# Performance work log

Hardware: AMD Instinct MI355X
Metric: run time of the kernel (lower is better)

## Reference

```python
import jax, jax.numpy as jnp
import numpy as np
from jax import lax

# Shared Conv2d [1,1] + BN + ReLU is represented as a per-point affine (BN folded
# into conv weight/bias at eval) followed by ReLU, matching inference-mode math.

B, N1, N2, K = 8, 8192, 2048, 8
C1, C2 = 64, 128
MLP0, MLP1, MLP2 = 128, 128, 128  # mlp=[128,128], mlp2=[128]


def setup_inputs() -> dict:
    key = jax.random.key(0)
    ks = jax.random.split(key, 10)
    sc = lambda fan_in: 1.0 / np.sqrt(fan_in)
    return {
        "xyz1": jax.random.normal(ks[0], (B, N1, 3), jnp.float32),
        "xyz2": jax.random.normal(ks[1], (B, N2, 3), jnp.float32),
        "feat1": jax.random.normal(ks[2], (B, N1, C1), jnp.float32),
        "feat2": jax.random.normal(ks[3], (B, N2, C2), jnp.float32),
        "W0": jax.random.normal(ks[4], (C2 + 3, MLP0), jnp.float32) * sc(C2 + 3),
        "b0": jnp.zeros((MLP0,), jnp.float32),
        "W1": jax.random.normal(ks[5], (MLP0, MLP1), jnp.float32) * sc(MLP0),
        "b1": jnp.zeros((MLP1,), jnp.float32),
        "W2": jax.random.normal(ks[6], (MLP1 + C1, MLP2), jnp.float32) * sc(MLP1 + C1),
        "b2": jnp.zeros((MLP2,), jnp.float32),
    }


def _knn_idx(xyz1, xyz2, k):
    # squared distances (B, N1, N2); top-k nearest in xyz2 for each xyz1 point
    d2 = jnp.sum((xyz1[:, :, None, :] - xyz2[:, None, :, :]) ** 2, axis=-1)
    _, idx = lax.top_k(-d2, k)  # (B, N1, K)
    return idx


def _gather(src, idx):
    # src: (B, N2, C), idx: (B, N1, K) -> (B, N1, K, C)
    return jax.vmap(lambda s, i: s[i])(src, idx)


def reference(xyz1, xyz2, feat1, feat2, W0, b0, W1, b1, W2, b2):
    idx = _knn_idx(xyz1, xyz2, K)
    xyz2_g = _gather(xyz2, idx)            # (B, N1, K, 3)
    feat2_g = _gather(feat2, idx)          # (B, N1, K, C2)
    xyz_diff = xyz2_g - xyz1[:, :, None, :]
    net = jnp.concatenate([feat2_g, xyz_diff], axis=-1)  # (B, N1, K, C2+3)
    net = jax.nn.relu(net @ W0 + b0)
    net = jax.nn.relu(net @ W1 + b1)       # (B, N1, K, MLP1)
    pooled = jnp.max(net, axis=2)          # max pooling over neighbors
    cat = jnp.concatenate([pooled, feat1], axis=-1)      # (B, N1, MLP1+C1)
    out = jax.nn.relu(cat @ W2 + b2)       # (B, N1, MLP2)
    return out
```

## Files before the change

### kernel.cpp

```cpp
#include <hip/hip_runtime.h>
#include <hip/hip_bf16.h>

constexpr int B_  = 8;
constexpr int N1_ = 8192;
constexpr int N2_ = 2048;
constexpr int K_  = 8;

typedef short bf16x8 __attribute__((ext_vector_type(8)));
typedef float f32x4  __attribute__((ext_vector_type(4)));
typedef float f32x2  __attribute__((ext_vector_type(2)));

__device__ __forceinline__ short f2b(float x) {
    __hip_bfloat16 h = __float2bfloat16(x);
    return *reinterpret_cast<short*>(&h);
}

#define CASF(a, b) { const float _lo = fminf(a, b); \
                     const float _hi = fmaxf(a, b); \
                     (a) = _lo; (b) = _hi; }

__global__ __launch_bounds__(256) void prep_all(
    const float* __restrict__ feat2, short* __restrict__ feat2b,
    const float* __restrict__ W0, const float* __restrict__ W1,
    const float* __restrict__ W2, const float* __restrict__ xyz2,
    short* __restrict__ W0T, short* __restrict__ W1T, short* __restrict__ W2T,
    float* __restrict__ xp) {
    if (blockIdx.x < 2048) {
        const int i = blockIdx.x * 256 + threadIdx.x;
        const float4 v = ((const float4*)feat2)[i];
        uint2 o;
        o.x = (unsigned short)f2b(v.x) | ((unsigned)(unsigned short)f2b(v.y) << 16);
        o.y = (unsigned short)f2b(v.z) | ((unsigned)(unsigned short)f2b(v.w) << 16);
        ((uint2*)feat2b)[i] = o;
        return;
    }
    int i = (blockIdx.x - 2048) * 256 + threadIdx.x;
    if (i < 128 * 160) {
        const int n = i / 160, k = i % 160;
        W0T[i] = (k < 131) ? f2b(W0[k * 128 + n]) : (short)0;
        return;
    }
    i -= 128 * 160;
    if (i < 128 * 128) {
        const int n = i >> 7, k = i & 127;
        W1T[i] = f2b(W1[k * 128 + n]);
        return;
    }
    i -= 128 * 128;
    if (i < 128 * 192) {
        const int n = i / 192, k = i % 192;
        W2T[i] = f2b(W2[k * 128 + n]);
        return;
    }
    i -= 128 * 192;
    const int b = i >> 11, j = i & 2047;
    const float* src = xyz2 + ((size_t)b * N2_ + j) * 3;
    float* dst = xp + (size_t)b * 3 * N2_ + j;
    dst[0]        = src[0];
    dst[N2_]      = src[1];
    dst[2 * N2_]  = src[2];
}

constexpr int LCAP = 76;

__global__ __launch_bounds__(256) void knn_lazy(const float* __restrict__ xyz1,
                                                const float* __restrict__ xp,
                                                int* __restrict__ idx) {
    __shared__ __align__(16) unsigned short sMem[78 * 256];
    float* sD = (float*)sMem;
    int*   sI = (int*)sMem + 64 * 33;

    const int b = blockIdx.y;
    const int lane = threadIdx.x & 63;
    const int s = threadIdx.x >> 6;
    const int tid = threadIdx.x;
    const int n = blockIdx.x * 64 + lane;

    const float* q = xyz1 + ((size_t)b * N1_ + n) * 3;
    const float qx = q[0], qy = q[1], qz = q[2];
    const float* xs = xp + (size_t)b * 3 * N2_ + s * 512;
    const float* ys = xs + N2_;
    const float* zs = xs + 2 * N2_;

    float bd[K_];
#pragma unroll
    for (int t = 0; t < K_; ++t) bd[t] = 3.0e38f;
    int cnt = 0;

    const f32x2 qx2 = {qx, qx}, qy2 = {qy, qy}, qz2 = {qz, qz};

    for (int j0 = 0; j0 < 512; j0 += 8) {
        const float4 X0 = *(const float4*)(xs + j0);
        const float4 X1 = *(const float4*)(xs + j0 + 4);
        const float4 Y0 = *(const float4*)(ys + j0);
        const float4 Y1 = *(const float4*)(ys + j0 + 4);
        const float4 Z0 = *(const float4*)(zs + j0);
        const float4 Z1 = *(const float4*)(zs + j0 + 4);
        float xf[8];
        {
            f32x2 dx, dy, dz, d;
            dx = qx2 - f32x2{X0.x, X0.y}; dy = qy2 - f32x2{Y0.x, Y0.y}; dz = qz2 - f32x2{Z0.x, Z0.y};
            d = dx * dx + dy * dy + dz * dz; xf[0] = d.x; xf[1] = d.y;
            dx = qx2 - f32x2{X0.z, X0.w}; dy = qy2 - f32x2{Y0.z, Y0.w}; dz = qz2 - f32x2{Z0.z, Z0.w};
            d = dx * dx + dy * dy + dz * dz; xf[2] = d.x; xf[3] = d.y;
            dx = qx2 - f32x2{X1.x, X1.y}; dy = qy2 - f32x2{Y1.x, Y1.y}; dz = qz2 - f32x2{Z1.x, Z1.y};
            d = dx * dx + dy * dy + dz * dz; xf[4] = d.x; xf[5] = d.y;
            dx = qx2 - f32x2{X1.z, X1.w}; dy = qy2 - f32x2{Y1.z, Y1.w}; dz = qz2 - f32x2{Z1.z, Z1.w};
            d = dx * dx + dy * dy + dz * dz; xf[6] = d.x; xf[7] = d.y;
        }
        const float thr = bd[K_ - 1] * 1.0000038f;
#pragma unroll
        for (int u = 0; u < 8; ++u) {
            const bool acc = xf[u] < thr;
            if (acc) {
                const int capped = cnt < LCAP ? cnt : LCAP;
                sMem[capped * 256 + tid] = (unsigned short)(j0 + u);
                cnt++;
            }
        }
        CASF(xf[0], xf[1]); CASF(xf[2], xf[3]); CASF(xf[4], xf[5]); CASF(xf[6], xf[7]);
        CASF(xf[0], xf[2]); CASF(xf[1], xf[3]); CASF(xf[4], xf[6]); CASF(xf[5], xf[7]);
        CASF(xf[1], xf[2]); CASF(xf[5], xf[6]); CASF(xf[0], xf[4]); CASF(xf[3], xf[7]);
        CASF(xf[1], xf[5]); CASF(xf[2], xf[6]);
        CASF(xf[1], xf[4]); CASF(xf[3], xf[6]);
        CASF(xf[2], xf[4]); CASF(xf[3], xf[5]);
        CASF(xf[3], xf[4]);
        float t0 = fminf(bd[0], xf[7]);
        float t1 = fminf(bd[1], xf[6]);
        float t2 = fminf(bd[2], xf[5]);
        float t3 = fminf(bd[3], xf[4]);
        float t4 = fminf(bd[4], xf[3]);
        float t5 = fminf(bd[5], xf[2]);
        float t6 = fminf(bd[6], xf[1]);
        float t7 = fminf(bd[7], xf[0]);
        CASF(t0, t4); CASF(t1, t5); CASF(t2, t6); CASF(t3, t7);
        CASF(t0, t2); CASF(t1, t3); CASF(t4, t6); CASF(t5, t7);
        CASF(t0, t1); CASF(t2, t3); CASF(t4, t5); CASF(t6, t7);
        bd[0] = t0; bd[1] = t1; bd[2] = t2; bd[3] = t3;
        bd[4] = t4; bd[5] = t5; bd[6] = t6; bd[7] = t7;
    }

    float rd[K_];
    int   ri[K_];
#pragma unroll
    for (int t = 0; t < K_; ++t) { rd[t] = 3.0e38f; ri[t] = 0; }
    const int m = cnt < LCAP ? cnt : LCAP;
    for (int t = 0;; ++t) {
        const bool act = t < m;
        if (!__any(act)) break;
        if (act) {
#pragma clang fp contract(off)
            const int jl = sMem[t * 256 + tid];
            const float dx = qx - xs[jl];
            const float dy = qy - ys[jl];
            const float dz = qz - zs[jl];
            const float dx2 = dx * dx;
            const float dy2 = dy * dy;
            const float dz2 = dz * dz;
            const float d2 = (dx2 + dy2) + dz2;
            if (d2 < rd[K_ - 1]) {
                rd[K_ - 1] = d2; ri[K_ - 1] = s * 512 + jl;
#pragma unroll
                for (int t2 = K_ - 1; t2 >= 1; --t2) {
                    if (rd[t2] < rd[t2 - 1]) {
                        float td = rd[t2]; rd[t2] = rd[t2 - 1]; rd[t2 - 1] = td;
                        int   ti = ri[t2]; ri[t2] = ri[t2 - 1]; ri[t2 - 1] = ti;
                    }
                }
            }
        }
    }

    if (__any(cnt > LCAP)) {
        if (cnt > LCAP) {
#pragma unroll
            for (int t = 0; t < K_; ++t) { rd[t] = 3.0e38f; ri[t] = 0; }
            for (int j = 0; j < 512; ++j) {
#pragma clang fp contract(off)
                const float dx = qx - xs[j];
                const float dy = qy - ys[j];
                const float dz = qz - zs[j];
                const float dx2 = dx * dx;
                const float dy2 = dy * dy;
                const float dz2 = dz * dz;
                const float d2 = (dx2 + dy2) + dz2;
                if (d2 < rd[K_ - 1]) {
                    rd[K_ - 1] = d2; ri[K_ - 1] = s * 512 + j;
#pragma unroll
                    for (int t2 = K_ - 1; t2 >= 1; --t2) {
                        if (rd[t2] < rd[t2 - 1]) {
                            float td = rd[t2]; rd[t2] = rd[t2 - 1]; rd[t2 - 1] = td;
                            int   ti = ri[t2]; ri[t2] = ri[t2 - 1]; ri[t2 - 1] = ti;
                        }
                    }
                }
            }
        }
    }

    __syncthreads();
#pragma unroll
    for (int t = 0; t < K_; ++t) {
        sD[lane * 33 + s * 8 + t] = rd[t];
        sI[lane * 33 + s * 8 + t] = ri[t];
    }
    __syncthreads();

    if (tid < 64) {
        const int qq = tid;
        int h[4] = {0, 0, 0, 0};
        const int base = (b * N1_ + n) * K_;
#pragma unroll
        for (int t = 0; t < K_; ++t) {
            float best = 3.1e38f;
            int   bidx = 0, bs = 0;
#pragma unroll
            for (int ss = 0; ss < 4; ++ss) {
                if (h[ss] < 8) {
                    const float d = sD[qq * 33 + ss * 8 + h[ss]];
                    if (d < best) { best = d; bidx = sI[qq * 33 + ss * 8 + h[ss]]; bs = ss; }
                }
            }
#pragma unroll
            for (int ss = 0; ss < 4; ++ss) h[ss] += (ss == bs) ? 1 : 0;
            idx[base + t] = bidx;
        }
    }
}

__global__ __launch_bounds__(256, 4) void fused_mfma(
    const float* __restrict__ xyz1, const float* __restrict__ xyz2,
    const float* __restrict__ feat1,
    const float* __restrict__ b0, const float* __restrict__ b1,
    const float* __restrict__ b2,
    const short* __restrict__ feat2b, const short* __restrict__ W0T,
    const short* __restrict__ W1T, const short* __restrict__ W2T,
    const int* __restrict__ idx, float* __restrict__ out) {
    __shared__ __align__(16) short sA[128 * 136 + 128 * 8];
    short* sXyz = sA + 128 * 136;
    short* sCat = sA;

    const int bid = blockIdx.x;
    const int b = bid & 7;
    const int n0 = (bid >> 3) * 16;
    const int tid = threadIdx.x;

    const float4 f1v = *(const float4*)(feat1 + ((size_t)b * N1_ + n0 + (tid >> 4)) * 64 + (tid & 15) * 4);

    {
        const int row = tid >> 1, half = tid & 1;
        const int p = row >> 3, kk = row & 7;
        const int n = n0 + p;
        const int j = idx[((size_t)b * N1_ + n) * K_ + kk];
        const uint4* src = (const uint4*)(feat2b + ((size_t)(b * N2_ + j)) * 128 + half * 64);
        uint4* dst = (uint4*)(sA + row * 136 + half * 64);
#pragma unroll
        for (int t = 0; t < 8; ++t) dst[t] = src[t];
        if (half == 0) {
            const float dx = xyz2[((size_t)b * N2_ + j) * 3 + 0] - xyz1[((size_t)b * N1_ + n) * 3 + 0];
            const float dy = xyz2[((size_t)b * N2_ + j) * 3 + 1] - xyz1[((size_t)b * N1_ + n) * 3 + 1];
            const float dz = xyz2[((size_t)b * N2_ + j) * 3 + 2] - xyz1[((size_t)b * N1_ + n) * 3 + 2];
            uint4 v;
            v.x = (unsigned short)f2b(dx) | ((unsigned)(unsigned short)f2b(dy) << 16);
            v.y = (unsigned short)f2b(dz);
            v.z = 0; v.w = 0;
            *(uint4*)(sXyz + row * 8) = v;
        }
    }
    __syncthreads();

    const int wave = tid >> 6, lane = tid & 63;
    const int q = lane >> 4, l15 = lane & 15;
    const int mBase = (wave & 1) * 64, nBase = (wave >> 1) * 64;

    const f32x4 zero4 = {0.f, 0.f, 0.f, 0.f};

    f32x4 acc[4][4];
#pragma unroll
    for (int mt = 0; mt < 4; ++mt)
#pragma unroll
        for (int nt = 0; nt < 4; ++nt) acc[mt][nt] = zero4;

    for (int ks = 0; ks < 4; ++ks) {
        bf16x8 af[4], bf[4];
#pragma unroll
        for (int mt = 0; mt < 4; ++mt)
            af[mt] = *(const bf16x8*)(sA + (mBase + mt * 16 + l15) * 136 + ks * 32 + q * 8);
#pragma unroll
        for (int nt = 0; nt < 4; ++nt)
            bf[nt] = *(const bf16x8*)(W0T + (nBase + nt * 16 + l15) * 160 + ks * 32 + q * 8);
#pragma unroll
        for (int mt = 0; mt < 4; ++mt)
#pragma unroll
            for (int nt = 0; nt < 4; ++nt)
                acc[mt][nt] = __builtin_amdgcn_mfma_f32_16x16x32_bf16(af[mt], bf[nt], acc[mt][nt], 0, 0, 0);
    }
    {
        bf16x8 af[4], bf[4];
#pragma unroll
        for (int mt = 0; mt < 4; ++mt)
            af[mt] = *(const bf16x8*)(sXyz + (mBase + mt * 16 + l15) * 8);
#pragma unroll
        for (int nt = 0; nt < 4; ++nt)
            bf[nt] = *(const bf16x8*)(W0T + (nBase + nt * 16 + l15) * 160 + 128 + q * 8);
#pragma unroll
        for (int mt = 0; mt < 4; ++mt)
#pragma unroll
            for (int nt = 0; nt < 4; ++nt)
                acc[mt][nt] = __builtin_amdgcn_mfma_f32_16x16x32_bf16(af[mt], bf[nt], acc[mt][nt], 0, 0, 0);
    }

    float b0v[4];
#pragma unroll
    for (int nt = 0; nt < 4; ++nt) b0v[nt] = b0[nBase + nt * 16 + l15];
    __syncthreads();
#pragma unroll
    for (int mt = 0; mt < 4; ++mt)
#pragma unroll
        for (int nt = 0; nt < 4; ++nt)
#pragma unroll
            for (int r = 0; r < 4; ++r) {
                const int row = mBase + mt * 16 + q * 4 + r;
                const int col = nBase + nt * 16 + l15;
                sA[row * 136 + col] = f2b(fmaxf(acc[mt][nt][r] + b0v[nt], 0.0f));
            }
    __syncthreads();

    f32x4 acc2[4][4];
#pragma unroll
    for (int mt = 0; mt < 4; ++mt)
#pragma unroll
        for (int nt = 0; nt < 4; ++nt) acc2[mt][nt] = zero4;

    for (int ks = 0; ks < 4; ++ks) {
        bf16x8 af[4], bf[4];
#pragma unroll
        for (int mt = 0; mt < 4; ++mt)
            af[mt] = *(const bf16x8*)(sA + (mBase + mt * 16 + l15) * 136 + ks * 32 + q * 8);
#pragma unroll
        for (int nt = 0; nt < 4; ++nt)
            bf[nt] = *(const bf16x8*)(W1T + (nBase + nt * 16 + l15) * 128 + ks * 32 + q * 8);
#pragma unroll
        for (int mt = 0; mt < 4; ++mt)
#pragma unroll
            for (int nt = 0; nt < 4; ++nt)
                acc2[mt][nt] = __builtin_amdgcn_mfma_f32_16x16x32_bf16(af[mt], bf[nt], acc2[mt][nt], 0, 0, 0);
    }

    float b1v[4];
#pragma unroll
    for (int nt = 0; nt < 4; ++nt) b1v[nt] = b1[nBase + nt * 16 + l15];

    __syncthreads();

#pragma unroll
    for (int mt = 0; mt < 4; ++mt)
#pragma unroll
        for (int nt = 0; nt < 4; ++nt) {
            float vm = fmaxf(acc2[mt][nt][0] + b1v[nt], 0.0f);
#pragma unroll
            for (int r = 1; r < 4; ++r) vm = fmaxf(vm, acc2[mt][nt][r] + b1v[nt]);
            const float other = __shfl_xor(vm, 16);
            const float pool = fmaxf(vm, other);
            if ((q & 1) == 0) {
                const int pp = (mBase >> 3) + mt * 2 + (q >> 1);
                sCat[pp * 200 + nBase + nt * 16 + l15] = f2b(pool);
            }
        }
    {
        const int p = tid >> 4;
        const int c4 = (tid & 15) * 4;
        uint2 w;
        w.x = (unsigned short)f2b(f1v.x) | ((unsigned)(unsigned short)f2b(f1v.y) << 16);
        w.y = (unsigned short)f2b(f1v.z) | ((unsigned)(unsigned short)f2b(f1v.w) << 16);
        *(uint2*)(sCat + p * 200 + 128 + c4) = w;
    }
    __syncthreads();

    f32x4 acc3[2];
    acc3[0] = zero4; acc3[1] = zero4;
    const int nB2 = wave * 32;
    for (int ks = 0; ks < 6; ++ks) {
        const bf16x8 a2 = *(const bf16x8*)(sCat + l15 * 200 + ks * 32 + q * 8);
#pragma unroll
        for (int nt = 0; nt < 2; ++nt) {
            const bf16x8 b2f = *(const bf16x8*)(W2T + (nB2 + nt * 16 + l15) * 192 + ks * 32 + q * 8);
            acc3[nt] = __builtin_amdgcn_mfma_f32_16x16x32_bf16(a2, b2f, acc3[nt], 0, 0, 0);
        }
    }
    float b2v[2];
#pragma unroll
    for (int nt = 0; nt < 2; ++nt) b2v[nt] = b2[nB2 + nt * 16 + l15];
#pragma unroll
    for (int nt = 0; nt < 2; ++nt)
#pragma unroll
        for (int r = 0; r < 4; ++r) {
            const int p = q * 4 + r;
            const int col = nB2 + nt * 16 + l15;
            out[((size_t)(b * N1_ + n0 + p)) * 128 + col] = fmaxf(acc3[nt][r] + b2v[nt], 0.0f);
        }
}

extern "C" void kernel_launch(void* const* d_in, const int* in_sizes, int n_in,
                              void* d_out, int out_size, void* d_ws, size_t ws_size,
                              hipStream_t stream) {
    const float* xyz1  = (const float*)d_in[0];
    const float* xyz2  = (const float*)d_in[1];
    const float* feat1 = (const float*)d_in[2];
    const float* feat2 = (const float*)d_in[3];
    const float* W0    = (const float*)d_in[4];
    const float* b0    = (const float*)d_in[5];
    const float* W1    = (const float*)d_in[6];
    const float* b1    = (const float*)d_in[7];
    const float* W2    = (const float*)d_in[8];
    const float* b2    = (const float*)d_in[9];
    float* out = (float*)d_out;

    char* ws = (char*)d_ws;
    int*    idx    = (int*)(ws + 0);
    short*  feat2b = (short*)(ws + 2097152);
    short*  W0T    = (short*)(ws + 6291456);
    short*  W1T    = (short*)(ws + 6332416);
    short*  W2T    = (short*)(ws + 6365184);
    float*  xp     = (float*)(ws + 6414336);

    prep_all<<<2352, 256, 0, stream>>>(feat2, feat2b, W0, W1, W2, xyz2,
                                       W0T, W1T, W2T, xp);
    knn_lazy<<<dim3(N1_ / 64, B_), 256, 0, stream>>>(xyz1, xp, idx);
    fused_mfma<<<dim3(8 * (N1_ / 16)), 256, 0, stream>>>(xyz1, xyz2, feat1, b0, b1, b2,
                                                         feat2b, W0T, W1T, W2T, idx, out);
}
```

Measured before the change: 312.2 us.

## Software-pipeline neighbor gathers across four point tiles per block

Each fused MLP block now handles four 16-point tiles instead of one. The next tile's gathered feat2 rows, xyz differences and feat1 are prefetched into registers while the current tile's MFMA chain runs, then written to shared memory after a barrier. Biases and indices are loaded once per block. The aim is to hide global gather latency behind compute and amortize block setup, at the cost of higher register pressure (launch bounds lowered to 3 blocks) and a quarter as many blocks.

```diff
diff --git a/kernel.cpp b/kernel.cpp
--- a/kernel.cpp
+++ b/kernel.cpp
@@ -228,7 +228,9 @@
     }
 }
 
-__global__ __launch_bounds__(256, 4) void fused_mfma(
+struct Pref { uint4 pf[8]; float dx, dy, dz; float4 f1; };
+
+__global__ __launch_bounds__(256, 3) void fused_mfma(
     const float* __restrict__ xyz1, const float* __restrict__ xyz2,
     const float* __restrict__ feat1,
     const float* __restrict__ b0, const float* __restrict__ b1,
@@ -242,163 +244,197 @@
 
     const int bid = blockIdx.x;
     const int b = bid & 7;
-    const int n0 = (bid >> 3) * 16;
+    const int n0b = (bid >> 3) * 64;
     const int tid = threadIdx.x;
-
-    const float4 f1v = *(const float4*)(feat1 + ((size_t)b * N1_ + n0 + (tid >> 4)) * 64 + (tid & 15) * 4);
-
-    {
-        const int row = tid >> 1, half = tid & 1;
-        const int p = row >> 3, kk = row & 7;
-        const int n = n0 + p;
-        const int j = idx[((size_t)b * N1_ + n) * K_ + kk];
-        const uint4* src = (const uint4*)(feat2b + ((size_t)(b * N2_ + j)) * 128 + half * 64);
-        uint4* dst = (uint4*)(sA + row * 136 + half * 64);
-#pragma unroll
-        for (int t = 0; t < 8; ++t) dst[t] = src[t];
-        if (half == 0) {
-            const float dx = xyz2[((size_t)b * N2_ + j) * 3 + 0] - xyz1[((size_t)b * N1_ + n) * 3 + 0];
-            const float dy = xyz2[((size_t)b * N2_ + j) * 3 + 1] - xyz1[((size_t)b * N1_ + n) * 3 + 1];
-            const float dz = xyz2[((size_t)b * N2_ + j) * 3 + 2] - xyz1[((size_t)b * N1_ + n) * 3 + 2];
-            uint4 v;
-            v.x = (unsigned short)f2b(dx) | ((unsigned)(unsigned short)f2b(dy) << 16);
-            v.y = (unsigned short)f2b(dz);
-            v.z = 0; v.w = 0;
-            *(uint4*)(sXyz + row * 8) = v;
-        }
-    }
-    __syncthreads();
-
     const int wave = tid >> 6, lane = tid & 63;
     const int q = lane >> 4, l15 = lane & 15;
     const int mBase = (wave & 1) * 64, nBase = (wave >> 1) * 64;
-
+    const int row = tid >> 1, half = tid & 1;
+    const int prow = row >> 3, kk = row & 7;
     const f32x4 zero4 = {0.f, 0.f, 0.f, 0.f};
 
-    f32x4 acc[4][4];
-#pragma unroll
-    for (int mt = 0; mt < 4; ++mt)
-#pragma unroll
-        for (int nt = 0; nt < 4; ++nt) acc[mt][nt] = zero4;
-
-    for (int ks = 0; ks < 4; ++ks) {
-        bf16x8 af[4], bf[4];
+    float b0v[4], b1v[4], b2v[2];
+#pragma unroll
+    for (int nt = 0; nt < 4; ++nt) b0v[nt] = b0[nBase + nt * 16 + l15];
+#pragma unroll
+    for (int nt = 0; nt < 4; ++nt) b1v[nt] = b1[nBase + nt * 16 + l15];
+    const int nB2 = wave * 32;
+#pragma unroll
+    for (int nt = 0; nt < 2; ++nt) b2v[nt] = b2[nB2 + nt * 16 + l15];
+
+    int j4[4];
+#pragma unroll
+    for (int it = 0; it < 4; ++it)
+        j4[it] = idx[((size_t)b * N1_ + n0b + it * 16 + prow) * K_ + kk];
+
+    auto ISSUE = [&](Pref& p, int it) {
+        const int n_ = n0b + it * 16 + prow;
+        const int j_ = j4[it];
+        const uint4* src = (const uint4*)(feat2b + ((size_t)(b * N2_ + j_)) * 128 + half * 64);
+#pragma unroll
+        for (int t = 0; t < 8; ++t) p.pf[t] = src[t];
+        if (half == 0) {
+            p.dx = xyz2[((size_t)b * N2_ + j_) * 3 + 0] - xyz1[((size_t)b * N1_ + n_) * 3 + 0];
+            p.dy = xyz2[((size_t)b * N2_ + j_) * 3 + 1] - xyz1[((size_t)b * N1_ + n_) * 3 + 1];
+            p.dz = xyz2[((size_t)b * N2_ + j_) * 3 + 2] - xyz1[((size_t)b * N1_ + n_) * 3 + 2];
+        }
+        p.f1 = *(const float4*)(feat1 + ((size_t)b * N1_ + n0b + it * 16 + (tid >> 4)) * 64 + (tid & 15) * 4);
+    };
+
+    auto WRITE = [&](const Pref& p) {
+        uint4* dst = (uint4*)(sA + row * 136 + half * 64);
+#pragma unroll
+        for (int t = 0; t < 8; ++t) dst[t] = p.pf[t];
+        if (half == 0) {
+            uint4 v;
+            v.x = (unsigned short)f2b(p.dx) | ((unsigned)(unsigned short)f2b(p.dy) << 16);
+            v.y = (unsigned short)f2b(p.dz);
+            v.z = 0; v.w = 0;
+            *(uint4*)(sXyz + row * 8) = v;
+        }
+    };
+
+    auto COMPUTE = [&](int it, float4 f1v) {
+        const int n0 = n0b + it * 16;
+        f32x4 acc[4][4];
 #pragma unroll
         for (int mt = 0; mt < 4; ++mt)
-            af[mt] = *(const bf16x8*)(sA + (mBase + mt * 16 + l15) * 136 + ks * 32 + q * 8);
-#pragma unroll
-        for (int nt = 0; nt < 4; ++nt)
-            bf[nt] = *(const bf16x8*)(W0T + (nBase + nt * 16 + l15) * 160 + ks * 32 + q * 8);
+#pragma unroll
+            for (int nt = 0; nt < 4; ++nt) acc[mt][nt] = zero4;
+
+        for (int ks = 0; ks < 4; ++ks) {
+            bf16x8 af[4], bf[4];
+#pragma unroll
+            for (int mt = 0; mt < 4; ++mt)
+                af[mt] = *(const bf16x8*)(sA + (mBase + mt * 16 + l15) * 136 + ks * 32 + q * 8);
+#pragma unroll
+            for (int nt = 0; nt < 4; ++nt)
+                bf[nt] = *(const bf16x8*)(W0T + (nBase + nt * 16 + l15) * 160 + ks * 32 + q * 8);
+#pragma unroll
+            for (int mt = 0; mt < 4; ++mt)
+#pragma unroll
+                for (int nt = 0; nt < 4; ++nt)
+                    acc[mt][nt] = __builtin_amdgcn_mfma_f32_16x16x32_bf16(af[mt], bf[nt], acc[mt][nt], 0, 0, 0);
+        }
+        {
+            bf16x8 af[4], bf[4];
+#pragma unroll
+            for (int mt = 0; mt < 4; ++mt)
+                af[mt] = *(const bf16x8*)(sXyz + (mBase + mt * 16 + l15) * 8);
+#pragma unroll
+            for (int nt = 0; nt < 4; ++nt)
+                bf[nt] = *(const bf16x8*)(W0T + (nBase + nt * 16 + l15) * 160 + 128 + q * 8);
+#pragma unroll
+            for (int mt = 0; mt < 4; ++mt)
+#pragma unroll
+                for (int nt = 0; nt < 4; ++nt)
+                    acc[mt][nt] = __builtin_amdgcn_mfma_f32_16x16x32_bf16(af[mt], bf[nt], acc[mt][nt], 0, 0, 0);
+        }
+
+        __syncthreads();
 #pragma unroll
         for (int mt = 0; mt < 4; ++mt)
 #pragma unroll
             for (int nt = 0; nt < 4; ++nt)
-                acc[mt][nt] = __builtin_amdgcn_mfma_f32_16x16x32_bf16(af[mt], bf[nt], acc[mt][nt], 0, 0, 0);
-    }
-    {
-        bf16x8 af[4], bf[4];
+#pragma unroll
+                for (int r = 0; r < 4; ++r) {
+                    const int rr = mBase + mt * 16 + q * 4 + r;
+                    const int col = nBase + nt * 16 + l15;
+                    sA[rr * 136 + col] = f2b(fmaxf(acc[mt][nt][r] + b0v[nt], 0.0f));
+                }
+        __syncthreads();
+
+        f32x4 acc2[4][4];
 #pragma unroll
         for (int mt = 0; mt < 4; ++mt)
-            af[mt] = *(const bf16x8*)(sXyz + (mBase + mt * 16 + l15) * 8);
-#pragma unroll
-        for (int nt = 0; nt < 4; ++nt)
-            bf[nt] = *(const bf16x8*)(W0T + (nBase + nt * 16 + l15) * 160 + 128 + q * 8);
+#pragma unroll
+            for (int nt = 0; nt < 4; ++nt) acc2[mt][nt] = zero4;
+
+        for (int ks = 0; ks < 4; ++ks) {
+            bf16x8 af[4], bf[4];
+#pragma unroll
+            for (int mt = 0; mt < 4; ++mt)
+                af[mt] = *(const bf16x8*)(sA + (mBase + mt * 16 + l15) * 136 + ks * 32 + q * 8);
+#pragma unroll
+            for (int nt = 0; nt < 4; ++nt)
+                bf[nt] = *(const bf16x8*)(W1T + (nBase + nt * 16 + l15) * 128 + ks * 32 + q * 8);
+#pragma unroll
+            for (int mt = 0; mt < 4; ++mt)
+#pragma unroll
+                for (int nt = 0; nt < 4; ++nt)
+                    acc2[mt][nt] = __builtin_amdgcn_mfma_f32_16x16x32_bf16(af[mt], bf[nt], acc2[mt][nt], 0, 0, 0);
+        }
+
+        __syncthreads();
+
 #pragma unroll
         for (int mt = 0; mt < 4; ++mt)
 #pragma unroll
-            for (int nt = 0; nt < 4; ++nt)
-                acc[mt][nt] = __builtin_amdgcn_mfma_f32_16x16x32_bf16(af[mt], bf[nt], acc[mt][nt], 0, 0, 0);
-    }
-
-    float b0v[4];
-#pragma unroll
-    for (int nt = 0; nt < 4; ++nt) b0v[nt] = b0[nBase + nt * 16 + l15];
-    __syncthreads();
-#pragma unroll
-    for (int mt = 0; mt < 4; ++mt)
-#pragma unroll
-        for (int nt = 0; nt < 4; ++nt)
+            for (int nt = 0; nt < 4; ++nt) {
+                float vm = fmaxf(acc2[mt][nt][0] + b1v[nt], 0.0f);
+#pragma unroll
+                for (int r = 1; r < 4; ++r) vm = fmaxf(vm, acc2[mt][nt][r] + b1v[nt]);
+                const float other = __shfl_xor(vm, 16);
+                const float pool = fmaxf(vm, other);
+                if ((q & 1) == 0) {
+                    const int pp = (mBase >> 3) + mt * 2 + (q >> 1);
+                    sCat[pp * 200 + nBase + nt * 16 + l15] = f2b(pool);
+                }
+            }
+        {
+            const int p = tid >> 4;
+            const int c4 = (tid & 15) * 4;
+            uint2 w;
+            w.x = (unsigned short)f2b(f1v.x) | ((unsigned)(unsigned short)f2b(f1v.y) << 16);
+            w.y = (unsigned short)f2b(f1v.z) | ((unsigned)(unsigned short)f2b(f1v.w) << 16);
+            *(uint2*)(sCat + p * 200 + 128 + c4) = w;
+        }
+        __syncthreads();
+
+        f32x4 acc3[2];
+        acc3[0] = zero4; acc3[1] = zero4;
+        for (int ks = 0; ks < 6; ++ks) {
+            const bf16x8 a2 = *(const bf16x8*)(sCat + l15 * 200 + ks * 32 + q * 8);
+#pragma unroll
+            for (int nt = 0; nt < 2; ++nt) {
+                const bf16x8 b2f = *(const bf16x8*)(W2T + (nB2 + nt * 16 + l15) * 192 + ks * 32 + q * 8);
+                acc3[nt] = __builtin_amdgcn_mfma_f32_16x16x32_bf16(a2, b2f, acc3[nt], 0, 0, 0);
+            }
+        }
+#pragma unroll
+        for (int nt = 0; nt < 2; ++nt)
 #pragma unroll
             for (int r = 0; r < 4; ++r) {
-                const int row = mBase + mt * 16 + q * 4 + r;
-                const int col = nBase + nt * 16 + l15;
-                sA[row * 136 + col] = f2b(fmaxf(acc[mt][nt][r] + b0v[nt], 0.0f));
-            }
-    __syncthreads();
-
-    f32x4 acc2[4][4];
-#pragma unroll
-    for (int mt = 0; mt < 4; ++mt)
-#pragma unroll
-        for (int nt = 0; nt < 4; ++nt) acc2[mt][nt] = zero4;
-
-    for (int ks = 0; ks < 4; ++ks) {
-        bf16x8 af[4], bf[4];
-#pragma unroll
-        for (int mt = 0; mt < 4; ++mt)
-            af[mt] = *(const bf16x8*)(sA + (mBase + mt * 16 + l15) * 136 + ks * 32 + q * 8);
-#pragma unroll
-        for (int nt = 0; nt < 4; ++nt)
-            bf[nt] = *(const bf16x8*)(W1T + (nBase + nt * 16 + l15) * 128 + ks * 32 + q * 8);
-#pragma unroll
-        for (int mt = 0; mt < 4; ++mt)
-#pragma unroll
-            for (int nt = 0; nt < 4; ++nt)
-                acc2[mt][nt] = __builtin_amdgcn_mfma_f32_16x16x32_bf16(af[mt], bf[nt], acc2[mt][nt], 0, 0, 0);
-    }
-
-    float b1v[4];
-#pragma unroll
-    for (int nt = 0; nt < 4; ++nt) b1v[nt] = b1[nBase + nt * 16 + l15];
-
-    __syncthreads();
-
-#pragma unroll
-    for (int mt = 0; mt < 4; ++mt)
-#pragma unroll
-        for (int nt = 0; nt < 4; ++nt) {
-            float vm = fmaxf(acc2[mt][nt][0] + b1v[nt], 0.0f);
-#pragma unroll
-            for (int r = 1; r < 4; ++r) vm = fmaxf(vm, acc2[mt][nt][r] + b1v[nt]);
-            const float other = __shfl_xor(vm, 16);
-            const float pool = fmaxf(vm, other);
-            if ((q & 1) == 0) {
-                const int pp = (mBase >> 3) + mt * 2 + (q >> 1);
-                sCat[pp * 200 + nBase + nt * 16 + l15] = f2b(pool);
-            }
-        }
-    {
-        const int p = tid >> 4;
-        const int c4 = (tid & 15) * 4;
-        uint2 w;
-        w.x = (unsigned short)f2b(f1v.x) | ((unsigned)(unsigned short)f2b(f1v.y) << 16);
-        w.y = (unsigned short)f2b(f1v.z) | ((unsigned)(unsigned short)f2b(f1v.w) << 16);
-        *(uint2*)(sCat + p * 200 + 128 + c4) = w;
-    }
-    __syncthreads();
-
-    f32x4 acc3[2];
-    acc3[0] = zero4; acc3[1] = zero4;
-    const int nB2 = wave * 32;
-    for (int ks = 0; ks < 6; ++ks) {
-        const bf16x8 a2 = *(const bf16x8*)(sCat + l15 * 200 + ks * 32 + q * 8);
-#pragma unroll
-        for (int nt = 0; nt < 2; ++nt) {
-            const bf16x8 b2f = *(const bf16x8*)(W2T + (nB2 + nt * 16 + l15) * 192 + ks * 32 + q * 8);
-            acc3[nt] = __builtin_amdgcn_mfma_f32_16x16x32_bf16(a2, b2f, acc3[nt], 0, 0, 0);
-        }
-    }
-    float b2v[2];
-#pragma unroll
-    for (int nt = 0; nt < 2; ++nt) b2v[nt] = b2[nB2 + nt * 16 + l15];
-#pragma unroll
-    for (int nt = 0; nt < 2; ++nt)
-#pragma unroll
-        for (int r = 0; r < 4; ++r) {
-            const int p = q * 4 + r;
-            const int col = nB2 + nt * 16 + l15;
-            out[((size_t)(b * N1_ + n0 + p)) * 128 + col] = fmaxf(acc3[nt][r] + b2v[nt], 0.0f);
-        }
+                const int p = q * 4 + r;
+                const int col = nB2 + nt * 16 + l15;
+                out[((size_t)(b * N1_ + n0 + p)) * 128 + col] = fmaxf(acc3[nt][r] + b2v[nt], 0.0f);
+            }
+    };
+
+    Pref pA, pB;
+    ISSUE(pA, 0);
+    WRITE(pA);
+    __syncthreads();
+
+    ISSUE(pB, 1);
+    COMPUTE(0, pA.f1);
+    __syncthreads();
+    WRITE(pB);
+    __syncthreads();
+
+    ISSUE(pA, 2);
+    COMPUTE(1, pB.f1);
+    __syncthreads();
+    WRITE(pA);
+    __syncthreads();
+
+    ISSUE(pB, 3);
+    COMPUTE(2, pA.f1);
+    __syncthreads();
+    WRITE(pB);
+    __syncthreads();
+
+    COMPUTE(3, pB.f1);
 }
 
 extern "C" void kernel_launch(void* const* d_in, const int* in_sizes, int n_in,
@@ -427,6 +463,6 @@
     prep_all<<<2352, 256, 0, stream>>>(feat2, feat2b, W0, W1, W2, xyz2,
                                        W0T, W1T, W2T, xp);
     knn_lazy<<<dim3(N1_ / 64, B_), 256, 0, stream>>>(xyz1, xp, idx);
-    fused_mfma<<<dim3(8 * (N1_ / 16)), 256, 0, stream>>>(xyz1, xyz2, feat1, b0, b1, b2,
+    fused_mfma<<<dim3(8 * (N1_ / 64)), 256, 0, stream>>>(xyz1, xyz2, feat1, b0, b1, b2,
                                                          feat2b, W0T, W1T, W2T, idx, out);
 }
```

After: 426.9 us. +36.8%, slower.

## Merge prep and kNN kernels, reading interleaved xyz2 directly

Applied to the files above, without the earlier changes.

Folds the bf16 conversion and weight transposes into the kNN kernel as extra blocks, removing one kernel launch and the xyz2 SoA transpose buffer. The kNN loop now reads AoS xyz2 with six float4 loads per 8 points instead of planar x/y/z loads, and uses scalar distance math instead of packed f32x2. Block indexing interleaves batches, so consecutive blocks work on different batches. This saves a launch and a transpose pass, at the cost of possibly less efficient loads and the loss of packed math in the hot loop.

```diff
diff --git a/kernel.cpp b/kernel.cpp
--- a/kernel.cpp
+++ b/kernel.cpp
@@ -8,7 +8,6 @@
 
 typedef short bf16x8 __attribute__((ext_vector_type(8)));
 typedef float f32x4  __attribute__((ext_vector_type(4)));
-typedef float f32x2  __attribute__((ext_vector_type(2)));
 
 __device__ __forceinline__ short f2b(float x) {
     __hip_bfloat16 h = __float2bfloat16(x);
@@ -19,94 +18,87 @@
                      const float _hi = fmaxf(a, b); \
                      (a) = _lo; (b) = _hi; }
 
-__global__ __launch_bounds__(256) void prep_all(
-    const float* __restrict__ feat2, short* __restrict__ feat2b,
+constexpr int LCAP = 76;
+
+__global__ __launch_bounds__(256) void prep_knn(
+    const float* __restrict__ xyz1, const float* __restrict__ xyz2,
+    const float* __restrict__ feat2,
     const float* __restrict__ W0, const float* __restrict__ W1,
-    const float* __restrict__ W2, const float* __restrict__ xyz2,
-    short* __restrict__ W0T, short* __restrict__ W1T, short* __restrict__ W2T,
-    float* __restrict__ xp) {
-    if (blockIdx.x < 2048) {
-        const int i = blockIdx.x * 256 + threadIdx.x;
-        const float4 v = ((const float4*)feat2)[i];
-        uint2 o;
-        o.x = (unsigned short)f2b(v.x) | ((unsigned)(unsigned short)f2b(v.y) << 16);
-        o.y = (unsigned short)f2b(v.z) | ((unsigned)(unsigned short)f2b(v.w) << 16);
-        ((uint2*)feat2b)[i] = o;
-        return;
-    }
-    int i = (blockIdx.x - 2048) * 256 + threadIdx.x;
-    if (i < 128 * 160) {
-        const int n = i / 160, k = i % 160;
-        W0T[i] = (k < 131) ? f2b(W0[k * 128 + n]) : (short)0;
-        return;
-    }
-    i -= 128 * 160;
-    if (i < 128 * 128) {
-        const int n = i >> 7, k = i & 127;
-        W1T[i] = f2b(W1[k * 128 + n]);
-        return;
-    }
-    i -= 128 * 128;
-    if (i < 128 * 192) {
+    const float* __restrict__ W2,
+    int* __restrict__ idx, short* __restrict__ feat2b,
+    short* __restrict__ W0T, short* __restrict__ W1T, short* __restrict__ W2T) {
+    const int tid = threadIdx.x;
+
+    if (blockIdx.x >= 1024) {
+        int i = (blockIdx.x - 1024) * 256 + tid;
+        if (i < 2048 * 256) {
+            const float4 v = ((const float4*)feat2)[i];
+            uint2 o;
+            o.x = (unsigned short)f2b(v.x) | ((unsigned)(unsigned short)f2b(v.y) << 16);
+            o.y = (unsigned short)f2b(v.z) | ((unsigned)(unsigned short)f2b(v.w) << 16);
+            ((uint2*)feat2b)[i] = o;
+            return;
+        }
+        i -= 2048 * 256;
+        if (i < 128 * 160) {
+            const int n = i / 160, k = i % 160;
+            W0T[i] = (k < 131) ? f2b(W0[k * 128 + n]) : (short)0;
+            return;
+        }
+        i -= 128 * 160;
+        if (i < 128 * 128) {
+            const int n = i >> 7, k = i & 127;
+            W1T[i] = f2b(W1[k * 128 + n]);
+            return;
+        }
+        i -= 128 * 128;
         const int n = i / 192, k = i % 192;
         W2T[i] = f2b(W2[k * 128 + n]);
         return;
     }
-    i -= 128 * 192;
-    const int b = i >> 11, j = i & 2047;
-    const float* src = xyz2 + ((size_t)b * N2_ + j) * 3;
-    float* dst = xp + (size_t)b * 3 * N2_ + j;
-    dst[0]        = src[0];
-    dst[N2_]      = src[1];
-    dst[2 * N2_]  = src[2];
-}
-
-constexpr int LCAP = 76;
-
-__global__ __launch_bounds__(256) void knn_lazy(const float* __restrict__ xyz1,
-                                                const float* __restrict__ xp,
-                                                int* __restrict__ idx) {
+
     __shared__ __align__(16) unsigned short sMem[78 * 256];
     float* sD = (float*)sMem;
     int*   sI = (int*)sMem + 64 * 33;
 
-    const int b = blockIdx.y;
-    const int lane = threadIdx.x & 63;
-    const int s = threadIdx.x >> 6;
-    const int tid = threadIdx.x;
-    const int n = blockIdx.x * 64 + lane;
+    const int b = blockIdx.x & 7;
+    const int t64 = blockIdx.x >> 3;
+    const int lane = tid & 63;
+    const int s = tid >> 6;
+    const int n = t64 * 64 + lane;
 
     const float* q = xyz1 + ((size_t)b * N1_ + n) * 3;
     const float qx = q[0], qy = q[1], qz = q[2];
-    const float* xs = xp + (size_t)b * 3 * N2_ + s * 512;
-    const float* ys = xs + N2_;
-    const float* zs = xs + 2 * N2_;
+    const float* P = xyz2 + ((size_t)b * N2_ + s * 512) * 3;
 
     float bd[K_];
 #pragma unroll
     for (int t = 0; t < K_; ++t) bd[t] = 3.0e38f;
     int cnt = 0;
 
-    const f32x2 qx2 = {qx, qx}, qy2 = {qy, qy}, qz2 = {qz, qz};
-
     for (int j0 = 0; j0 < 512; j0 += 8) {
-        const float4 X0 = *(const float4*)(xs + j0);
-        const float4 X1 = *(const float4*)(xs + j0 + 4);
-        const float4 Y0 = *(const float4*)(ys + j0);
-        const float4 Y1 = *(const float4*)(ys + j0 + 4);
-        const float4 Z0 = *(const float4*)(zs + j0);
-        const float4 Z1 = *(const float4*)(zs + j0 + 4);
+        const float4 F0 = *(const float4*)(P + j0 * 3 + 0);
+        const float4 F1 = *(const float4*)(P + j0 * 3 + 4);
+        const float4 F2 = *(const float4*)(P + j0 * 3 + 8);
+        const float4 F3 = *(const float4*)(P + j0 * 3 + 12);
+        const float4 F4 = *(const float4*)(P + j0 * 3 + 16);
+        const float4 F5 = *(const float4*)(P + j0 * 3 + 20);
+        float px[8], py[8], pz[8];
+        px[0] = F0.x; py[0] = F0.y; pz[0] = F0.z;
+        px[1] = F0.w; py[1] = F1.x; pz[1] = F1.y;
+        px[2] = F1.z; py[2] = F1.w; pz[2] = F2.x;
+        px[3] = F2.y; py[3] = F2.z; pz[3] = F2.w;
+        px[4] = F3.x; py[4] = F3.y; pz[4] = F3.z;
+        px[5] = F3.w; py[5] = F4.x; pz[5] = F4.y;
+        px[6] = F4.z; py[6] = F4.w; pz[6] = F5.x;
+        px[7] = F5.y; py[7] = F5.z; pz[7] = F5.w;
         float xf[8];
-        {
-            f32x2 dx, dy, dz, d;
-            dx = qx2 - f32x2{X0.x, X0.y}; dy = qy2 - f32x2{Y0.x, Y0.y}; dz = qz2 - f32x2{Z0.x, Z0.y};
-            d = dx * dx + dy * dy + dz * dz; xf[0] = d.x; xf[1] = d.y;
-            dx = qx2 - f32x2{X0.z, X0.w}; dy = qy2 - f32x2{Y0.z, Y0.w}; dz = qz2 - f32x2{Z0.z, Z0.w};
-            d = dx * dx + dy * dy + dz * dz; xf[2] = d.x; xf[3] = d.y;
-            dx = qx2 - f32x2{X1.x, X1.y}; dy = qy2 - f32x2{Y1.x, Y1.y}; dz = qz2 - f32x2{Z1.x, Z1.y};
-            d = dx * dx + dy * dy + dz * dz; xf[4] = d.x; xf[5] = d.y;
-            dx = qx2 - f32x2{X1.z, X1.w}; dy = qy2 - f32x2{Y1.z, Y1.w}; dz = qz2 - f32x2{Z1.z, Z1.w};
-            d = dx * dx + dy * dy + dz * dz; xf[6] = d.x; xf[7] = d.y;
+#pragma unroll
+        for (int u = 0; u < 8; ++u) {
+            const float dx = qx - px[u];
+            const float dy = qy - py[u];
+            const float dz = qz - pz[u];
+            xf[u] = dx * dx + dy * dy + dz * dz;
         }
         const float thr = bd[K_ - 1] * 1.0000038f;
 #pragma unroll
@@ -151,9 +143,10 @@
         if (act) {
 #pragma clang fp contract(off)
             const int jl = sMem[t * 256 + tid];
-            const float dx = qx - xs[jl];
-            const float dy = qy - ys[jl];
-            const float dz = qz - zs[jl];
+            const float* pp = P + jl * 3;
+            const float dx = qx - pp[0];
+            const float dy = qy - pp[1];
+            const float dz = qz - pp[2];
             const float dx2 = dx * dx;
             const float dy2 = dy * dy;
             const float dz2 = dz * dz;
@@ -177,9 +170,10 @@
             for (int t = 0; t < K_; ++t) { rd[t] = 3.0e38f; ri[t] = 0; }
             for (int j = 0; j < 512; ++j) {
 #pragma clang fp contract(off)
-                const float dx = qx - xs[j];
-                const float dy = qy - ys[j];
-                const float dz = qz - zs[j];
+                const float* pp = P + j * 3;
+                const float dx = qx - pp[0];
+                const float dy = qy - pp[1];
+                const float dz = qz - pp[2];
                 const float dx2 = dx * dx;
                 const float dy2 = dy * dy;
                 const float dz2 = dz * dz;
@@ -209,7 +203,7 @@
     if (tid < 64) {
         const int qq = tid;
         int h[4] = {0, 0, 0, 0};
-        const int base = (b * N1_ + n) * K_;
+        const int base = (b * N1_ + t64 * 64 + qq) * K_;
 #pragma unroll
         for (int t = 0; t < K_; ++t) {
             float best = 3.1e38f;
@@ -422,11 +416,9 @@
     short*  W0T    = (short*)(ws + 6291456);
     short*  W1T    = (short*)(ws + 6332416);
     short*  W2T    = (short*)(ws + 6365184);
-    float*  xp     = (float*)(ws + 6414336);
-
-    prep_all<<<2352, 256, 0, stream>>>(feat2, feat2b, W0, W1, W2, xyz2,
-                                       W0T, W1T, W2T, xp);
-    knn_lazy<<<dim3(N1_ / 64, B_), 256, 0, stream>>>(xyz1, xp, idx);
+
+    prep_knn<<<3312, 256, 0, stream>>>(xyz1, xyz2, feat2, W0, W1, W2,
+                                       idx, feat2b, W0T, W1T, W2T);
     fused_mfma<<<dim3(8 * (N1_ / 16)), 256, 0, stream>>>(xyz1, xyz2, feat1, b0, b1, b2,
                                                          feat2b, W0T, W1T, W2T, idx, out);
 }
```

Result: faster. 302.0 us (-3.3%).
